# Optimization experiments

Hardware: AMD Instinct MI355X
Metric: run time of the kernel (lower is better)

Reference implementation:

```python
import jax, jax.numpy as jnp
import numpy as np

B = 8          # batch size (clouds)
NC = 2048      # coarse points per cloud (pos / x)
NF = 8192      # fine points per cloud (pos_skip / x_skip)
C = 256        # coarse feature dim
CS = 64        # skip feature dim
OUT = 256      # MLP output dim
K = 3          # knn_interpolate k (FPParams default)
EPS = 1e-16    # PyG clamp epsilon on squared distance


def setup_inputs() -> dict:
    key = jax.random.key(0)
    ks = jax.random.split(key, 8)
    x = jax.random.normal(ks[0], (B * NC, C), dtype=jnp.float32)
    pos = jax.random.normal(ks[1], (B * NC, 3), dtype=jnp.float32)
    x_skip = jax.random.normal(ks[2], (B * NF, CS), dtype=jnp.float32)
    pos_skip = jax.random.normal(ks[3], (B * NF, 3), dtype=jnp.float32)
    # contiguous, sorted batch assignments (standard PyG layout)
    batch = jnp.repeat(jnp.arange(B, dtype=jnp.int64), NC)
    batch_skip = jnp.repeat(jnp.arange(B, dtype=jnp.int64), NF)
    W1 = jax.random.normal(ks[4], (C + CS, OUT), dtype=jnp.float32) * (1.0 / np.sqrt(C + CS))
    b1 = jnp.zeros((OUT,), dtype=jnp.float32)
    W2 = jax.random.normal(ks[5], (OUT, OUT), dtype=jnp.float32) * (1.0 / np.sqrt(OUT))
    b2 = jnp.zeros((OUT,), dtype=jnp.float32)
    return {"x": x, "pos": pos, "batch": batch, "x_skip": x_skip,
            "pos_skip": pos_skip, "batch_skip": batch_skip,
            "W1": W1, "b1": b1, "W2": W2, "b2": b2}


def _knn_interpolate(x, pos, pos_skip):
    # x: [B*NC, C], pos: [B*NC, 3], pos_skip: [B*NF, 3]
    posb = pos.reshape(B, NC, 3)
    posf = pos_skip.reshape(B, NF, 3)
    xb = x.reshape(B, NC, -1)
    # squared pairwise distances per cloud: [B, NF, NC]
    d2 = jnp.sum((posf[:, :, None, :] - posb[:, None, :, :]) ** 2, axis=-1)
    neg_d2, idx = jax.lax.top_k(-d2, K)          # k nearest -> [B, NF, K]
    d2k = -neg_d2
    w = 1.0 / jnp.maximum(d2k, EPS)              # inverse squared-distance weights
    w = w / jnp.sum(w, axis=-1, keepdims=True)   # [B, NF, K]
    gathered = jax.vmap(lambda xv, iv: xv[iv])(xb, idx)  # [B, NF, K, C]
    out = jnp.sum(gathered * w[..., None], axis=2)       # [B, NF, C]
    return out.reshape(B * NF, -1)


def reference(x, pos, batch, x_skip, pos_skip, batch_skip, W1, b1, W2, b2):
    # 1) interpolate coarse features onto fine points (pos.shape[0] != pos_skip.shape[0])
    xi = _knn_interpolate(x, pos, pos_skip)        # [B*NF, C]
    # 2) concat skip features
    h = jnp.concatenate([xi, x_skip], axis=1)      # [B*NF, C+CS]
    # 3) MLP: Linear -> ReLU -> Linear -> ReLU
    h = jax.nn.relu(h @ W1 + b1)
    h = jax.nn.relu(h @ W2 + b2)
    return (h, pos_skip, batch_skip)
```

## Files before the change

kernel.cpp:

```cpp
#include <hip/hip_runtime.h>
#include <hip/hip_bf16.h>

#define BATCH 8
#define NC 2048
#define NF 8192
#define CDIM 256
#define CSKIP 64
#define OUTD 256
#define MTOT (BATCH*NF)
#define NCTOT (BATCH*NC)
#define NCHUNK 8
#define CHSZ (NC/NCHUNK)

typedef __attribute__((ext_vector_type(8))) short short8;
typedef __attribute__((ext_vector_type(4))) float floatx4;

static __device__ __forceinline__ ushort f2bf(float f) {
    union { float f; unsigned u; } v; v.f = f;
    unsigned r = v.u + 0x7fffu + ((v.u >> 16) & 1u);
    return (ushort)(r >> 16);
}
static __device__ __forceinline__ float bf2f(ushort u) {
    union { unsigned u; float f; } v; v.u = ((unsigned)u) << 16;
    return v.f;
}

#if defined(__has_builtin) && __has_builtin(__builtin_amdgcn_fmed3f)
#define MED3F(a, b, c) __builtin_amdgcn_fmed3f((a), (b), (c))
#else
static __device__ __forceinline__ float MED3F(float a, float b, float c) {
    return fmaxf(fminf(a, b), fminf(fmaxf(a, b), c));
}
#endif

#define TOP3_INS(d, jj, D0, D1, D2, I0, I1, I2)     \
    {                                               \
        bool c2 = (d) < D2, c1 = (d) < D1, c0 = (d) < D0; \
        I2 = c1 ? I1 : (c2 ? (jj) : I2);            \
        I1 = c0 ? I0 : (c1 ? (jj) : I1);            \
        I0 = c0 ? (jj) : I0;                        \
        D2 = MED3F(D1, D2, (d));                    \
        D1 = MED3F(D0, D1, (d));                    \
        D0 = fminf(D0, (d));                        \
    }

#define SEG0 1048576
#define SEG1 1048576
#define SEG5 16384
#define SEG6 (MTOT*3)
#define SEG7 MTOT
#define PREP_THREADS (SEG0+SEG1+SEG5+SEG6+SEG7)

__global__ __launch_bounds__(256) void prep_kernel(const float* __restrict__ x,
                                                   const float* __restrict__ x_skip,
                                                   const float* __restrict__ pos,
                                                   const float* __restrict__ pos_skip,
                                                   ushort* __restrict__ xb,
                                                   ushort* __restrict__ xsb,
                                                   float4* __restrict__ pos4,
                                                   float* __restrict__ out) {
    int t = blockIdx.x * 256 + threadIdx.x;
    if (t < SEG0) {
        float4 v = ((const float4*)x)[t];
        ushort4 p; p.x = f2bf(v.x); p.y = f2bf(v.y); p.z = f2bf(v.z); p.w = f2bf(v.w);
        ((ushort4*)xb)[t] = p;
        return;
    }
    t -= SEG0;
    if (t < SEG1) {
        float4 v = ((const float4*)x_skip)[t];
        ushort4 p; p.x = f2bf(v.x); p.y = f2bf(v.y); p.z = f2bf(v.z); p.w = f2bf(v.w);
        ((ushort4*)xsb)[t] = p;
        return;
    }
    t -= SEG1;
    if (t < SEG5) {
        float4 q;
        q.x = pos[t * 3 + 0]; q.y = pos[t * 3 + 1]; q.z = pos[t * 3 + 2]; q.w = 0.f;
        pos4[t] = q;
        return;
    }
    t -= SEG5;
    if (t < SEG6) {
        out[(size_t)MTOT * OUTD + t] = pos_skip[t];
        return;
    }
    t -= SEG6;
    if (t < SEG7) {
        out[(size_t)MTOT * OUTD + (size_t)MTOT * 3 + t] = (float)(t >> 13);
    }
}

__global__ __launch_bounds__(256) void prep_w(const float* __restrict__ W1,
                                              const float* __restrict__ W2,
                                              ushort* __restrict__ Bt1a,
                                              ushort* __restrict__ Bt1b,
                                              ushort* __restrict__ Bt2) {
    __shared__ ushort tile[64 * 65];
    int bid = blockIdx.x;
    const float* src; ushort* dst; int k0, n0, KD;
    if (bid < 16)      { src = W1;             dst = Bt1a; k0 = (bid >> 2) * 64; n0 = (bid & 3) * 64; KD = 256; }
    else if (bid < 20) { src = W1 + 256 * 256; dst = Bt1b; k0 = 0;               n0 = (bid - 16) * 64; KD = 64; }
    else               { int b2 = bid - 20; src = W2; dst = Bt2; k0 = (b2 >> 2) * 64; n0 = (b2 & 3) * 64; KD = 256; }
    int tx = threadIdx.x & 63, ty = threadIdx.x >> 6;
#pragma unroll
    for (int r = 0; r < 64; r += 4) {
        int k = r + ty;
        tile[k * 65 + tx] = f2bf(src[(size_t)(k0 + k) * 256 + n0 + tx]);
    }
    __syncthreads();
#pragma unroll
    for (int r = 0; r < 64; r += 4) {
        int n = r + ty;
        dst[(size_t)(n0 + n) * KD + k0 + tx] = tile[tx * 65 + n];
    }
}

__global__ __launch_bounds__(256) void knn_part(const float4* __restrict__ pos4,
                                                const float* __restrict__ pos_skip,
                                                int* __restrict__ pidx,
                                                float* __restrict__ pdst) {
    __shared__ float sx[CHSZ], sy[CHSZ], sz[CHSZ];
    int c = blockIdx.x & (NCHUNK - 1);
    int mA = (blockIdx.x >> 3) * 512 + threadIdx.x;
    int mB = mA + 256;
    int b = mA >> 13;
    int jbase = b * NC + c * CHSZ;

    float4 q0 = pos4[jbase + threadIdx.x];
    sx[threadIdx.x] = q0.x; sy[threadIdx.x] = q0.y; sz[threadIdx.x] = q0.z;
    float pxA = pos_skip[mA * 3 + 0];
    float pyA = pos_skip[mA * 3 + 1];
    float pzA = pos_skip[mA * 3 + 2];
    float pxB = pos_skip[mB * 3 + 0];
    float pyB = pos_skip[mB * 3 + 1];
    float pzB = pos_skip[mB * 3 + 2];
    __syncthreads();

    float dA0 = 1e30f, dA1 = 1e30f, dA2 = 1e30f;
    float dB0 = 1e30f, dB1 = 1e30f, dB2 = 1e30f;
    int iA0 = jbase, iA1 = jbase, iA2 = jbase;
    int iB0 = jbase, iB1 = jbase, iB2 = jbase;
#pragma unroll 2
    for (int j4 = 0; j4 < CHSZ; j4 += 4) {
        float4 qx = *(const float4*)&sx[j4];
        float4 qy = *(const float4*)&sy[j4];
        float4 qz = *(const float4*)&sz[j4];
#pragma unroll
        for (int u = 0; u < 4; ++u) {
            int jj = jbase + j4 + u;
            float ax = pxA - qx[u], ay = pyA - qy[u], az = pzA - qz[u];
            float dA = ax * ax + ay * ay + az * az;
            TOP3_INS(dA, jj, dA0, dA1, dA2, iA0, iA1, iA2);
            float bx = pxB - qx[u], by = pyB - qy[u], bz = pzB - qz[u];
            float dB = bx * bx + by * by + bz * bz;
            TOP3_INS(dB, jj, dB0, dB1, dB2, iB0, iB1, iB2);
        }
    }
    size_t baseA = ((size_t)c * MTOT + mA) * 3;
    pdst[baseA + 0] = dA0; pdst[baseA + 1] = dA1; pdst[baseA + 2] = dA2;
    pidx[baseA + 0] = iA0; pidx[baseA + 1] = iA1; pidx[baseA + 2] = iA2;
    size_t baseB = ((size_t)c * MTOT + mB) * 3;
    pdst[baseB + 0] = dB0; pdst[baseB + 1] = dB1; pdst[baseB + 2] = dB2;
    pidx[baseB + 0] = iB0; pidx[baseB + 1] = iB1; pidx[baseB + 2] = iB2;
}

__global__ __launch_bounds__(64) void knn_merge(const int* __restrict__ pidx,
                                                const float* __restrict__ pdst,
                                                int* __restrict__ idxw,
                                                float* __restrict__ wgt) {
    int m = blockIdx.x * 64 + threadIdx.x;
    float d0 = 1e30f, d1 = 1e30f, d2 = 1e30f;
    int i0 = 0, i1 = 0, i2 = 0;
#pragma unroll
    for (int c = 0; c < NCHUNK; ++c) {
        size_t base = ((size_t)c * MTOT + m) * 3;
#pragma unroll
        for (int s = 0; s < 3; ++s) {
            float d = pdst[base + s];
            int jj = pidx[base + s];
            TOP3_INS(d, jj, d0, d1, d2, i0, i1, i2);
        }
    }
    float w0 = 1.0f / fmaxf(d0, 1e-16f);
    float w1 = 1.0f / fmaxf(d1, 1e-16f);
    float w2 = 1.0f / fmaxf(d2, 1e-16f);
    float inv = 1.0f / (w0 + w1 + w2);
    idxw[m * 3 + 0] = i0;  wgt[m * 3 + 0] = w0 * inv;
    idxw[m * 3 + 1] = i1;  wgt[m * 3 + 1] = w1 * inv;
    idxw[m * 3 + 2] = i2;  wgt[m * 3 + 2] = w2 * inv;
}

#define GW_STRIDE 72
__global__ __launch_bounds__(256) void gemm_G(const ushort* __restrict__ A,
                                              const ushort* __restrict__ Bt,
                                              ushort* __restrict__ Gb) {
    __shared__ ushort wB[256 * GW_STRIDE];
    int tid = threadIdx.x;
    int wave = tid >> 6, lane = tid & 63;
    int m0 = blockIdx.x * 64 + wave * 16;
    int lrow = lane & 15;
    int ko = (lane >> 4) * 8;

    floatx4 acc[16];
#pragma unroll
    for (int i = 0; i < 16; ++i) acc[i] = (floatx4){0.f, 0.f, 0.f, 0.f};

    for (int s = 0; s < 4; ++s) {
        if (s) __syncthreads();
        for (int cch = tid; cch < 2048; cch += 256) {
            int n = cch >> 3, koff = (cch & 7) * 8;
            *(short8*)&wB[n * GW_STRIDE + koff] = *(const short8*)(Bt + n * 256 + s * 64 + koff);
        }
        __syncthreads();
        const ushort* ar = A + (size_t)(m0 + lrow) * 256 + s * 64 + ko;
#pragma unroll
        for (int k0 = 0; k0 < 64; k0 += 32) {
            short8 af = *(const short8*)(ar + k0);
#pragma unroll
            for (int nt = 0; nt < 16; ++nt) {
                short8 bf = *(const short8*)&wB[(nt * 16 + lrow) * GW_STRIDE + k0 + ko];
                acc[nt] = __builtin_amdgcn_mfma_f32_16x16x32_bf16(af, bf, acc[nt], 0, 0, 0);
            }
        }
    }
    int rbase = (lane >> 4) * 4;
#pragma unroll
    for (int nt = 0; nt < 16; ++nt) {
        int n = nt * 16 + lrow;
#pragma unroll
        for (int r = 0; r < 4; ++r)
            Gb[(size_t)(m0 + rbase + r) * 256 + n] = f2bf(acc[nt][r]);
    }
}

#define LDS_STRIDE 264
#define WB_STRIDE 72
__global__ __launch_bounds__(256) void fused_kernel(const ushort* __restrict__ xsb,
                                                    const ushort* __restrict__ Bt1b,
                                                    const ushort* __restrict__ Gb,
                                                    const int* __restrict__ idxw,
                                                    const float* __restrict__ wgt,
                                                    const float* __restrict__ b1,
                                                    const ushort* __restrict__ Bt2,
                                                    const float* __restrict__ b2,
                                                    float* __restrict__ out) {
    __shared__ ushort h1t[4][16 * LDS_STRIDE];
    __shared__ ushort wB[256 * WB_STRIDE];
    __shared__ int   sIdx[4][48];
    __shared__ float sWgt[4][48];
    int tid = threadIdx.x;
    int wave = tid >> 6, lane = tid & 63;
    int m0 = blockIdx.x * 64 + wave * 16;
    int lrow = lane & 15;
    int ko = (lane >> 4) * 8;
    int rbase = (lane >> 4) * 4;

    if (lane < 48) {
        sIdx[wave][lane] = idxw[m0 * 3 + lane];
        sWgt[wave][lane] = wgt[m0 * 3 + lane];
    }

    const ushort4* Gv = (const ushort4*)Gb;
    const int*   si = sIdx[wave];
    const float* sw = sWgt[wave];
    ushort4 g[4][3];
#define GATHER(slot, i) {                                         \
        int a0 = si[(i) * 3 + 0];                                 \
        int a1 = si[(i) * 3 + 1];                                 \
        int a2 = si[(i) * 3 + 2];                                 \
        g[slot][0] = Gv[(size_t)a0 * 64 + lane];                  \
        g[slot][1] = Gv[(size_t)a1 * 64 + lane];                  \
        g[slot][2] = Gv[(size_t)a2 * 64 + lane]; }

    GATHER(0, 0) GATHER(1, 1) GATHER(2, 2) GATHER(3, 3)

    for (int cch = tid; cch < 2048; cch += 256) {
        int n = cch >> 3, koff = (cch & 7) * 8;
        *(short8*)&wB[n * WB_STRIDE + koff] = *(const short8*)(Bt1b + n * 64 + koff);
    }
    __syncthreads();

    floatx4 acc[16];
#pragma unroll
    for (int i = 0; i < 16; ++i) acc[i] = (floatx4){0.f, 0.f, 0.f, 0.f};
    {
        const ushort* arow = xsb + (size_t)(m0 + lrow) * 64 + ko;
#pragma unroll
        for (int k0 = 0; k0 < 64; k0 += 32) {
            short8 af = *(const short8*)(arow + k0);
#pragma unroll
            for (int nt = 0; nt < 16; ++nt) {
                short8 bf = *(const short8*)&wB[(nt * 16 + lrow) * WB_STRIDE + k0 + ko];
                acc[nt] = __builtin_amdgcn_mfma_f32_16x16x32_bf16(af, bf, acc[nt], 0, 0, 0);
            }
        }
    }

    ushort* ht = h1t[wave];
#pragma unroll
    for (int nt = 0; nt < 16; ++nt) {
        int n = nt * 16 + lrow;
#pragma unroll
        for (int r = 0; r < 4; ++r)
            ht[(rbase + r) * LDS_STRIDE + n] = f2bf(acc[nt][r]);
    }

    {
        float4 bv = ((const float4*)b1)[lane];
#define COMBINE(i) {                                              \
        int s = (i) & 3;                                          \
        float w0 = sw[(i) * 3 + 0], w1 = sw[(i) * 3 + 1], w2 = sw[(i) * 3 + 2]; \
        ushort4 sv = *(const ushort4*)(ht + (i) * LDS_STRIDE + 4 * lane); \
        float4 h;                                                 \
        h.x = fmaxf(bf2f(sv.x) + w0 * bf2f(g[s][0].x) + w1 * bf2f(g[s][1].x) + w2 * bf2f(g[s][2].x) + bv.x, 0.f); \
        h.y = fmaxf(bf2f(sv.y) + w0 * bf2f(g[s][0].y) + w1 * bf2f(g[s][1].y) + w2 * bf2f(g[s][2].y) + bv.y, 0.f); \
        h.z = fmaxf(bf2f(sv.z) + w0 * bf2f(g[s][0].z) + w1 * bf2f(g[s][1].z) + w2 * bf2f(g[s][2].z) + bv.z, 0.f); \
        h.w = fmaxf(bf2f(sv.w) + w0 * bf2f(g[s][0].w) + w1 * bf2f(g[s][1].w) + w2 * bf2f(g[s][2].w) + bv.w, 0.f); \
        ushort4 hp;                                               \
        hp.x = f2bf(h.x); hp.y = f2bf(h.y); hp.z = f2bf(h.z); hp.w = f2bf(h.w); \
        *(ushort4*)(ht + (i) * LDS_STRIDE + 4 * lane) = hp; }

#pragma unroll
        for (int i = 0; i < 12; ++i) { COMBINE(i); GATHER(i & 3, i + 4); }
#pragma unroll
        for (int i = 12; i < 16; ++i) { COMBINE(i); }
#undef GATHER
#undef COMBINE
    }

#pragma unroll
    for (int i = 0; i < 16; ++i) acc[i] = (floatx4){0.f, 0.f, 0.f, 0.f};
    for (int s = 0; s < 4; ++s) {
        __syncthreads();
        for (int cch = tid; cch < 2048; cch += 256) {
            int n = cch >> 3, koff = (cch & 7) * 8;
            *(short8*)&wB[n * WB_STRIDE + koff] = *(const short8*)(Bt2 + n * 256 + s * 64 + koff);
        }
        __syncthreads();
        const ushort* ar = ht + lrow * LDS_STRIDE + s * 64 + ko;
#pragma unroll
        for (int k0 = 0; k0 < 64; k0 += 32) {
            short8 af = *(const short8*)(ar + k0);
#pragma unroll
            for (int nt = 0; nt < 16; ++nt) {
                short8 bf = *(const short8*)&wB[(nt * 16 + lrow) * WB_STRIDE + k0 + ko];
                acc[nt] = __builtin_amdgcn_mfma_f32_16x16x32_bf16(af, bf, acc[nt], 0, 0, 0);
            }
        }
    }
#pragma unroll
    for (int nt = 0; nt < 16; ++nt) {
        int n = nt * 16 + lrow;
        float bv2 = b2[n];
#pragma unroll
        for (int r = 0; r < 4; ++r) {
            float v = fmaxf(acc[nt][r] + bv2, 0.f);
            out[(size_t)(m0 + rbase + r) * OUTD + n] = v;
        }
    }
}

extern "C" void kernel_launch(void* const* d_in, const int* in_sizes, int n_in,
                              void* d_out, int out_size, void* d_ws, size_t ws_size,
                              hipStream_t stream) {
    const float* x        = (const float*)d_in[0];
    const float* pos      = (const float*)d_in[1];
    const float* x_skip   = (const float*)d_in[3];
    const float* pos_skip = (const float*)d_in[4];
    const float* W1       = (const float*)d_in[6];
    const float* b1       = (const float*)d_in[7];
    const float* W2       = (const float*)d_in[8];
    const float* b2       = (const float*)d_in[9];

    char* ws = (char*)d_ws;
    size_t off = 0;
    int*    idxw = (int*)(ws + off);    off += (size_t)MTOT * 3 * 4;
    float*  wgt  = (float*)(ws + off);  off += (size_t)MTOT * 3 * 4;
    ushort* xb   = (ushort*)(ws + off); off += (size_t)NCTOT * 256 * 2;
    ushort* xsb  = (ushort*)(ws + off); off += (size_t)MTOT * 64 * 2;
    ushort* Gb   = (ushort*)(ws + off); off += (size_t)NCTOT * 256 * 2;
    ushort* Bt1a = (ushort*)(ws + off); off += (size_t)256 * 256 * 2;
    ushort* Bt1b = (ushort*)(ws + off); off += (size_t)256 * 64 * 2;
    ushort* Bt2  = (ushort*)(ws + off); off += (size_t)256 * 256 * 2;
    float4* pos4 = (float4*)(ws + off); off += (size_t)(NCTOT + 4) * 16;
    float* out = (float*)d_out;
    int*   pidx = (int*)d_out;
    float* pdst = (float*)((char*)d_out + (size_t)NCHUNK * MTOT * 3 * 4);

    prep_kernel<<<(PREP_THREADS + 255) / 256, 256, 0, stream>>>(
        x, x_skip, pos, pos_skip, xb, xsb, pos4, out);
    prep_w<<<36, 256, 0, stream>>>(W1, W2, Bt1a, Bt1b, Bt2);
    knn_part<<<(MTOT / 512) * NCHUNK, 256, 0, stream>>>(pos4, pos_skip, pidx, pdst);
    knn_merge<<<MTOT / 64, 64, 0, stream>>>(pidx, pdst, idxw, wgt);
    gemm_G<<<NCTOT / 64, 256, 0, stream>>>(xb, Bt1a, Gb);
    fused_kernel<<<MTOT / 64, 256, 0, stream>>>(xsb, Bt1b, Gb, idxw, wgt, b1, Bt2, b2, out);
}
```

Baseline: 226.2 us.

## Merge prep/weight kernels, widen knn_part to 4 queries, co-launch merge with gemm_G

Folds the weight transpose/convert into the prep kernel and runs the knn merge as extra blocks of the gemm_G launch, cutting six launches to four. knn_part now handles four fine points per thread instead of two, so each shared-memory coarse load is reused more often and half as many blocks are launched. The costs are higher register pressure in knn_part and fewer blocks (512) to fill the GPU, plus a __syncthreads inside a branch of prep_kernel that relies on every thread of those blocks taking the same path.

```diff
diff --git a/kernel.cpp b/kernel.cpp
--- a/kernel.cpp
+++ b/kernel.cpp
@@ -49,16 +49,23 @@
 #define SEG5 16384
 #define SEG6 (MTOT*3)
 #define SEG7 MTOT
-#define PREP_THREADS (SEG0+SEG1+SEG5+SEG6+SEG7)
+#define SEGW (36*256)
+#define PREP_THREADS (SEG0+SEG1+SEG5+SEG6+SEG7+SEGW)
 
 __global__ __launch_bounds__(256) void prep_kernel(const float* __restrict__ x,
                                                    const float* __restrict__ x_skip,
                                                    const float* __restrict__ pos,
                                                    const float* __restrict__ pos_skip,
+                                                   const float* __restrict__ W1,
+                                                   const float* __restrict__ W2,
                                                    ushort* __restrict__ xb,
                                                    ushort* __restrict__ xsb,
                                                    float4* __restrict__ pos4,
+                                                   ushort* __restrict__ Bt1a,
+                                                   ushort* __restrict__ Bt1b,
+                                                   ushort* __restrict__ Bt2,
                                                    float* __restrict__ out) {
+    __shared__ ushort tile[64 * 65];
     int t = blockIdx.x * 256 + threadIdx.x;
     if (t < SEG0) {
         float4 v = ((const float4*)x)[t];
@@ -88,31 +95,27 @@
     t -= SEG6;
     if (t < SEG7) {
         out[(size_t)MTOT * OUTD + (size_t)MTOT * 3 + t] = (float)(t >> 13);
-    }
-}
-
-__global__ __launch_bounds__(256) void prep_w(const float* __restrict__ W1,
-                                              const float* __restrict__ W2,
-                                              ushort* __restrict__ Bt1a,
-                                              ushort* __restrict__ Bt1b,
-                                              ushort* __restrict__ Bt2) {
-    __shared__ ushort tile[64 * 65];
-    int bid = blockIdx.x;
-    const float* src; ushort* dst; int k0, n0, KD;
-    if (bid < 16)      { src = W1;             dst = Bt1a; k0 = (bid >> 2) * 64; n0 = (bid & 3) * 64; KD = 256; }
-    else if (bid < 20) { src = W1 + 256 * 256; dst = Bt1b; k0 = 0;               n0 = (bid - 16) * 64; KD = 64; }
-    else               { int b2 = bid - 20; src = W2; dst = Bt2; k0 = (b2 >> 2) * 64; n0 = (b2 & 3) * 64; KD = 256; }
-    int tx = threadIdx.x & 63, ty = threadIdx.x >> 6;
-#pragma unroll
-    for (int r = 0; r < 64; r += 4) {
-        int k = r + ty;
-        tile[k * 65 + tx] = f2bf(src[(size_t)(k0 + k) * 256 + n0 + tx]);
-    }
-    __syncthreads();
-#pragma unroll
-    for (int r = 0; r < 64; r += 4) {
-        int n = r + ty;
-        dst[(size_t)(n0 + n) * KD + k0 + tx] = tile[tx * 65 + n];
+        return;
+    }
+    t -= SEG7;
+    if (t < SEGW) {
+        int bid = t >> 8;
+        int tx = t & 63, ty = (t >> 6) & 3;
+        const float* src; ushort* dst; int k0, n0, KD;
+        if (bid < 16)      { src = W1;             dst = Bt1a; k0 = (bid >> 2) * 64; n0 = (bid & 3) * 64; KD = 256; }
+        else if (bid < 20) { src = W1 + 256 * 256; dst = Bt1b; k0 = 0;               n0 = (bid - 16) * 64; KD = 64; }
+        else               { int b2 = bid - 20; src = W2; dst = Bt2; k0 = (b2 >> 2) * 64; n0 = (b2 & 3) * 64; KD = 256; }
+#pragma unroll
+        for (int r = 0; r < 64; r += 4) {
+            int k = r + ty;
+            tile[k * 65 + tx] = f2bf(src[(size_t)(k0 + k) * 256 + n0 + tx]);
+        }
+        __syncthreads();
+#pragma unroll
+        for (int r = 0; r < 64; r += 4) {
+            int n = r + ty;
+            dst[(size_t)(n0 + n) * KD + k0 + tx] = tile[tx * 65 + n];
+        }
     }
 }
 
@@ -122,25 +125,31 @@
                                                 float* __restrict__ pdst) {
     __shared__ float sx[CHSZ], sy[CHSZ], sz[CHSZ];
     int c = blockIdx.x & (NCHUNK - 1);
-    int mA = (blockIdx.x >> 3) * 512 + threadIdx.x;
-    int mB = mA + 256;
-    int b = mA >> 13;
+    int m0 = (blockIdx.x >> 3) * 1024 + threadIdx.x;
+    int b = m0 >> 13;
     int jbase = b * NC + c * CHSZ;
 
     float4 q0 = pos4[jbase + threadIdx.x];
     sx[threadIdx.x] = q0.x; sy[threadIdx.x] = q0.y; sz[threadIdx.x] = q0.z;
-    float pxA = pos_skip[mA * 3 + 0];
-    float pyA = pos_skip[mA * 3 + 1];
-    float pzA = pos_skip[mA * 3 + 2];
-    float pxB = pos_skip[mB * 3 + 0];
-    float pyB = pos_skip[mB * 3 + 1];
-    float pzB = pos_skip[mB * 3 + 2];
+
+    float px[4], py[4], pz[4];
+#pragma unroll
+    for (int p = 0; p < 4; ++p) {
+        int m = m0 + p * 256;
+        px[p] = pos_skip[m * 3 + 0];
+        py[p] = pos_skip[m * 3 + 1];
+        pz[p] = pos_skip[m * 3 + 2];
+    }
     __syncthreads();
 
-    float dA0 = 1e30f, dA1 = 1e30f, dA2 = 1e30f;
-    float dB0 = 1e30f, dB1 = 1e30f, dB2 = 1e30f;
-    int iA0 = jbase, iA1 = jbase, iA2 = jbase;
-    int iB0 = jbase, iB1 = jbase, iB2 = jbase;
+    float d0[4], d1[4], d2[4];
+    int i0[4], i1[4], i2[4];
+#pragma unroll
+    for (int p = 0; p < 4; ++p) {
+        d0[p] = 1e30f; d1[p] = 1e30f; d2[p] = 1e30f;
+        i0[p] = jbase; i1[p] = jbase; i2[p] = jbase;
+    }
+
 #pragma unroll 2
     for (int j4 = 0; j4 < CHSZ; j4 += 4) {
         float4 qx = *(const float4*)&sx[j4];
@@ -149,54 +158,56 @@
 #pragma unroll
         for (int u = 0; u < 4; ++u) {
             int jj = jbase + j4 + u;
-            float ax = pxA - qx[u], ay = pyA - qy[u], az = pzA - qz[u];
-            float dA = ax * ax + ay * ay + az * az;
-            TOP3_INS(dA, jj, dA0, dA1, dA2, iA0, iA1, iA2);
-            float bx = pxB - qx[u], by = pyB - qy[u], bz = pzB - qz[u];
-            float dB = bx * bx + by * by + bz * bz;
-            TOP3_INS(dB, jj, dB0, dB1, dB2, iB0, iB1, iB2);
-        }
-    }
-    size_t baseA = ((size_t)c * MTOT + mA) * 3;
-    pdst[baseA + 0] = dA0; pdst[baseA + 1] = dA1; pdst[baseA + 2] = dA2;
-    pidx[baseA + 0] = iA0; pidx[baseA + 1] = iA1; pidx[baseA + 2] = iA2;
-    size_t baseB = ((size_t)c * MTOT + mB) * 3;
-    pdst[baseB + 0] = dB0; pdst[baseB + 1] = dB1; pdst[baseB + 2] = dB2;
-    pidx[baseB + 0] = iB0; pidx[baseB + 1] = iB1; pidx[baseB + 2] = iB2;
-}
-
-__global__ __launch_bounds__(64) void knn_merge(const int* __restrict__ pidx,
-                                                const float* __restrict__ pdst,
-                                                int* __restrict__ idxw,
-                                                float* __restrict__ wgt) {
-    int m = blockIdx.x * 64 + threadIdx.x;
-    float d0 = 1e30f, d1 = 1e30f, d2 = 1e30f;
-    int i0 = 0, i1 = 0, i2 = 0;
-#pragma unroll
-    for (int c = 0; c < NCHUNK; ++c) {
+#pragma unroll
+            for (int p = 0; p < 4; ++p) {
+                float ax = px[p] - qx[u], ay = py[p] - qy[u], az = pz[p] - qz[u];
+                float d = ax * ax + ay * ay + az * az;
+                TOP3_INS(d, jj, d0[p], d1[p], d2[p], i0[p], i1[p], i2[p]);
+            }
+        }
+    }
+#pragma unroll
+    for (int p = 0; p < 4; ++p) {
+        int m = m0 + p * 256;
         size_t base = ((size_t)c * MTOT + m) * 3;
-#pragma unroll
-        for (int s = 0; s < 3; ++s) {
-            float d = pdst[base + s];
-            int jj = pidx[base + s];
-            TOP3_INS(d, jj, d0, d1, d2, i0, i1, i2);
-        }
-    }
-    float w0 = 1.0f / fmaxf(d0, 1e-16f);
-    float w1 = 1.0f / fmaxf(d1, 1e-16f);
-    float w2 = 1.0f / fmaxf(d2, 1e-16f);
-    float inv = 1.0f / (w0 + w1 + w2);
-    idxw[m * 3 + 0] = i0;  wgt[m * 3 + 0] = w0 * inv;
-    idxw[m * 3 + 1] = i1;  wgt[m * 3 + 1] = w1 * inv;
-    idxw[m * 3 + 2] = i2;  wgt[m * 3 + 2] = w2 * inv;
+        pdst[base + 0] = d0[p]; pdst[base + 1] = d1[p]; pdst[base + 2] = d2[p];
+        pidx[base + 0] = i0[p]; pidx[base + 1] = i1[p]; pidx[base + 2] = i2[p];
+    }
 }
 
 #define GW_STRIDE 72
-__global__ __launch_bounds__(256) void gemm_G(const ushort* __restrict__ A,
-                                              const ushort* __restrict__ Bt,
-                                              ushort* __restrict__ Gb) {
+__global__ __launch_bounds__(256) void mid_kernel(const ushort* __restrict__ A,
+                                                  const ushort* __restrict__ Bt,
+                                                  ushort* __restrict__ Gb,
+                                                  const int* __restrict__ pidx,
+                                                  const float* __restrict__ pdst,
+                                                  int* __restrict__ idxw,
+                                                  float* __restrict__ wgt) {
     __shared__ ushort wB[256 * GW_STRIDE];
     int tid = threadIdx.x;
+    if (blockIdx.x >= NCTOT / 64) {
+        int m = (blockIdx.x - NCTOT / 64) * 256 + tid;
+        float d0 = 1e30f, d1 = 1e30f, d2 = 1e30f;
+        int i0 = 0, i1 = 0, i2 = 0;
+#pragma unroll
+        for (int c = 0; c < NCHUNK; ++c) {
+            size_t base = ((size_t)c * MTOT + m) * 3;
+#pragma unroll
+            for (int s = 0; s < 3; ++s) {
+                float d = pdst[base + s];
+                int jj = pidx[base + s];
+                TOP3_INS(d, jj, d0, d1, d2, i0, i1, i2);
+            }
+        }
+        float w0 = 1.0f / fmaxf(d0, 1e-16f);
+        float w1 = 1.0f / fmaxf(d1, 1e-16f);
+        float w2 = 1.0f / fmaxf(d2, 1e-16f);
+        float inv = 1.0f / (w0 + w1 + w2);
+        idxw[m * 3 + 0] = i0;  wgt[m * 3 + 0] = w0 * inv;
+        idxw[m * 3 + 1] = i1;  wgt[m * 3 + 1] = w1 * inv;
+        idxw[m * 3 + 2] = i2;  wgt[m * 3 + 2] = w2 * inv;
+        return;
+    }
     int wave = tid >> 6, lane = tid & 63;
     int m0 = blockIdx.x * 64 + wave * 16;
     int lrow = lane & 15;
@@ -388,11 +399,10 @@
     int*   pidx = (int*)d_out;
     float* pdst = (float*)((char*)d_out + (size_t)NCHUNK * MTOT * 3 * 4);
 
-    prep_kernel<<<(PREP_THREADS + 255) / 256, 256, 0, stream>>>(
-        x, x_skip, pos, pos_skip, xb, xsb, pos4, out);
-    prep_w<<<36, 256, 0, stream>>>(W1, W2, Bt1a, Bt1b, Bt2);
-    knn_part<<<(MTOT / 512) * NCHUNK, 256, 0, stream>>>(pos4, pos_skip, pidx, pdst);
-    knn_merge<<<MTOT / 64, 64, 0, stream>>>(pidx, pdst, idxw, wgt);
-    gemm_G<<<NCTOT / 64, 256, 0, stream>>>(xb, Bt1a, Gb);
+    prep_kernel<<<PREP_THREADS / 256, 256, 0, stream>>>(
+        x, x_skip, pos, pos_skip, W1, W2, xb, xsb, pos4, Bt1a, Bt1b, Bt2, out);
+    knn_part<<<(MTOT / 1024) * NCHUNK, 256, 0, stream>>>(pos4, pos_skip, pidx, pdst);
+    mid_kernel<<<NCTOT / 64 + MTOT / 256, 256, 0, stream>>>(
+        xb, Bt1a, Gb, pidx, pdst, idxw, wgt);
     fused_kernel<<<MTOT / 64, 256, 0, stream>>>(xsb, Bt1b, Gb, idxw, wgt, b1, Bt2, b2, out);
 }
```

After: 248.1 us. 9.7% more time.
